# Performance work log

Measured on AMD Instinct MI355X. Metric: run time of the kernel, lower is better.

## Reference

```python
import jax, jax.numpy as jnp
import numpy as np

N = 50000      # nodes
E = 800000     # edges
F_NODE = 64    # num_node_features
F_EDGE = 16    # num_edge_features
C = 64         # out_channels
L = 3          # n_hidden_layers
G = 512        # num graphs in batch
NCLS = 10      # num_classes
EPS = 1e-5


def _lin_init(k, shape, fan_in):
    lim = 1.0 / np.sqrt(fan_in)
    return jax.random.uniform(k, shape, jnp.float32, -lim, lim)


def setup_inputs() -> dict:
    key = jax.random.key(0)
    ks = jax.random.split(key, 32)
    inp = {
        "x": jax.random.normal(ks[0], (N, F_NODE), jnp.float32),
        "edge_index": jax.random.randint(ks[1], (2, E), 0, N, jnp.int32),
        "batch": ((jnp.arange(N) * G) // N).astype(jnp.int32),  # sorted, covers all graphs
        "dropout": 0,
        "edge_attr": jax.random.uniform(ks[2], (E, F_EDGE), jnp.float32),
        # conv1: PDNConv(F_NODE, C, F_EDGE, F_EDGE). torch Linear layout [out,in].
        "c1_lw": _lin_init(ks[3], (C, F_NODE), F_NODE),
        "c1_w1": _lin_init(ks[4], (F_EDGE, F_EDGE), F_EDGE),
        "c1_b1": _lin_init(ks[5], (F_EDGE,), F_EDGE),
        "c1_w2": _lin_init(ks[6], (1, F_EDGE), F_EDGE),
        "c1_b2": _lin_init(ks[7], (1,), F_EDGE),
        # hidden_conv_1 / hidden_conv_2: L stacked PDNConv(C, C, F_EDGE, F_EDGE)
        "h1_lw": _lin_init(ks[8], (L, C, C), C),
        "h1_w1": _lin_init(ks[9], (L, F_EDGE, F_EDGE), F_EDGE),
        "h1_b1": _lin_init(ks[10], (L, F_EDGE), F_EDGE),
        "h1_w2": _lin_init(ks[11], (L, 1, F_EDGE), F_EDGE),
        "h1_b2": _lin_init(ks[12], (L, 1), F_EDGE),
        "h2_lw": _lin_init(ks[13], (L, C, C), C),
        "h2_w1": _lin_init(ks[14], (L, F_EDGE, F_EDGE), F_EDGE),
        "h2_b1": _lin_init(ks[15], (L, F_EDGE), F_EDGE),
        "h2_w2": _lin_init(ks[16], (L, 1, F_EDGE), F_EDGE),
        "h2_b2": _lin_init(ks[17], (L, 1), F_EDGE),
        # final classifier Linear(C, NCLS)
        "lin_w": _lin_init(ks[18], (NCLS, C), C),
        "lin_b": _lin_init(ks[19], (NCLS,), C),
    }
    return inp


def _pdn_conv(x, row, col, loop, edge_attr, lw, w1, b1, w2, b2):
    """PDNConv: edge-MLP weight -> add self loops -> gcn_norm -> gather-scale-scatter."""
    # edge weight MLP: Linear -> ReLU -> Linear -> Sigmoid, squeeze to [E]
    w = jax.nn.sigmoid(jnp.squeeze(jax.nn.relu(edge_attr @ w1.T + b1) @ w2.T + b2, -1))
    wf = jnp.concatenate([w, jnp.ones((x.shape[0],), x.dtype)])  # self-loop weight 1
    r = jnp.concatenate([row, loop])
    c = jnp.concatenate([col, loop])
    deg = jax.ops.segment_sum(wf, c, num_segments=x.shape[0])
    dis = jnp.where(deg > 0, 1.0 / jnp.sqrt(deg), 0.0)
    norm = dis[r] * wf * dis[c]                 # gcn_norm edge coefficients
    xl = x @ lw.T                                # node transform [N, C]
    msg = xl[r] * norm[:, None]                  # gather + scale [E+N, C]
    return jax.ops.segment_sum(msg, c, num_segments=x.shape[0])


def _batch_norm(x):
    # fresh BatchNorm each forward: weight=1, bias=0, training-mode batch stats
    mu = jnp.mean(x, axis=0)
    var = jnp.mean(jnp.square(x - mu), axis=0)  # biased var
    return (x - mu) * jax.lax.rsqrt(var + EPS)


def reference(x, edge_index, batch, dropout, edge_attr,
              c1_lw, c1_w1, c1_b1, c1_w2, c1_b2,
              h1_lw, h1_w1, h1_b1, h1_w2, h1_b2,
              h2_lw, h2_w1, h2_b1, h2_w2, h2_b2,
              lin_w, lin_b):
    row, col = edge_index[0], edge_index[1]
    loop = jnp.arange(x.shape[0], dtype=row.dtype)

    x = _pdn_conv(x, row, col, loop, edge_attr, c1_lw, c1_w1, c1_b1, c1_w2, c1_b2)
    x0 = x
    for i in range(L):
        x = jax.nn.relu(_batch_norm(x))
        x = _pdn_conv(x, row, col, loop, edge_attr,
                      h1_lw[i], h1_w1[i], h1_b1[i], h1_w2[i], h1_b2[i])
    x1 = x + x0
    x = x + x0
    for i in range(L):
        x = jax.nn.relu(_batch_norm(x))
        x = _pdn_conv(x, row, col, loop, edge_attr,
                      h2_lw[i], h2_w1[i], h2_b1[i], h2_w2[i], h2_b2[i])
    x2 = jax.nn.relu(x + x0 + x1)
    pooled = jax.ops.segment_max(x2, batch, num_segments=G)  # global max pool [G, C]
    # dropout p passed in is 0 / eval -> identity
    return pooled @ lin_w.T + lin_b
```

## Files before the change

kernel.cpp:

```cpp
#include <hip/hip_runtime.h>
#include <hip/hip_bf16.h>
#include <math.h>

#define NN 50000
#define NE 800000
#define FE 16
#define CC 64
#define NG 512
#define NCLS 10
#define NCONV 7
#define SCAN_B 49

struct MlpP { const float* w1; const float* b1; const float* w2; const float* b2; };
struct MlpAll { MlpP p[NCONV]; };

__device__ __forceinline__ int lowerb(const int* __restrict__ a, int n, int key) {
  int lo = 0, hi = n;
  while (lo < hi) { int m = (lo + hi) >> 1; if (a[m] < key) lo = m + 1; else hi = m; }
  return lo;
}

__global__ __launch_bounds__(256) void k_hist(const int* __restrict__ ecol, int* __restrict__ cnt) {
  int e = blockIdx.x * 256 + threadIdx.x;
  if (e < NE) atomicAdd(&cnt[ecol[e]], 1);
}

__global__ __launch_bounds__(1024) void k_scanA(const int* __restrict__ cnt, int* __restrict__ excl,
                                                int* __restrict__ bsum) {
  __shared__ int sc[1024];
  int t = threadIdx.x;
  int i = blockIdx.x * 1024 + t;
  int v = (i < NN) ? cnt[i] : 0;
  sc[t] = v;
  __syncthreads();
  for (int off = 1; off < 1024; off <<= 1) {
    int u = (t >= off) ? sc[t - off] : 0;
    __syncthreads();
    sc[t] += u;
    __syncthreads();
  }
  if (i < NN) excl[i] = sc[t] - v;
  if (t == 1023) bsum[blockIdx.x] = sc[1023];
}

__global__ void k_scanB(const int* __restrict__ bsum, int* __restrict__ boff) {
  int lane = threadIdx.x;
  int v = (lane < SCAN_B) ? bsum[lane] : 0;
  int own = v;
  for (int off = 1; off < 64; off <<= 1) {
    int u = __shfl_up(v, off);
    if (lane >= off) v += u;
  }
  if (lane < SCAN_B) boff[lane] = v - own;
}

__global__ __launch_bounds__(1024) void k_scanC(const int* __restrict__ excl, const int* __restrict__ boff,
                                                int* __restrict__ cptr, int* __restrict__ cursor) {
  int i = blockIdx.x * 1024 + threadIdx.x;
  if (i < NN) {
    int p = excl[i] + boff[blockIdx.x];
    cptr[i] = p;
    cursor[i] = p;
  }
  if (i == 0) cptr[NN] = NE;
}

__global__ __launch_bounds__(256) void k_scatter(
    const int* __restrict__ erow, const int* __restrict__ ecol,
    int* __restrict__ cursor, int* __restrict__ csrc, int* __restrict__ pos) {
  int e = blockIdx.x * 256 + threadIdx.x;
  if (e >= NE) return;
  int c = ecol[e];
  int p = atomicAdd(&cursor[c], 1);
  csrc[p] = erow[e];
  pos[e] = p;
}

__global__ __launch_bounds__(256) void k_mlp(
    const int* __restrict__ pos, const float* __restrict__ ea,
    float* __restrict__ wcsr8, MlpAll mw) {
  int e = blockIdx.x * 256 + threadIdx.x;
  if (e >= NE) return;
  float a[16];
  const float4* ea4 = reinterpret_cast<const float4*>(ea + (size_t)e * 16);
  float4 q0 = ea4[0], q1 = ea4[1], q2 = ea4[2], q3 = ea4[3];
  a[0]=q0.x; a[1]=q0.y; a[2]=q0.z; a[3]=q0.w;
  a[4]=q1.x; a[5]=q1.y; a[6]=q1.z; a[7]=q1.w;
  a[8]=q2.x; a[9]=q2.y; a[10]=q2.z; a[11]=q2.w;
  a[12]=q3.x; a[13]=q3.y; a[14]=q3.z; a[15]=q3.w;
  float wv[NCONV];
  #pragma unroll
  for (int j = 0; j < NCONV; ++j) {
    const float* w1 = mw.p[j].w1;
    const float* b1 = mw.p[j].b1;
    const float* w2 = mw.p[j].w2;
    float z = mw.p[j].b2[0];
    #pragma unroll
    for (int k = 0; k < 16; ++k) {
      float h = b1[k];
      #pragma unroll
      for (int m = 0; m < 16; ++m) h += a[m] * w1[k * 16 + m];
      h = h > 0.f ? h : 0.f;
      z += h * w2[k];
    }
    wv[j] = 1.f / (1.f + __expf(-z));
  }
  int p = pos[e];
  float4* dst = reinterpret_cast<float4*>(wcsr8 + (size_t)p * 8);
  dst[0] = make_float4(wv[0], wv[1], wv[2], wv[3]);
  dst[1] = make_float4(wv[4], wv[5], wv[6], 0.f);
}

__global__ __launch_bounds__(256) void k_deg(const float* __restrict__ wcsr8,
                                             const int* __restrict__ cptr,
                                             float* __restrict__ dis) {
  int n = blockIdx.x * 256 + threadIdx.x;
  if (n >= NN) return;
  int lo = cptr[n], hi = cptr[n + 1];
  float s0=0,s1=0,s2=0,s3=0,s4=0,s5=0,s6=0;
  for (int k = lo; k < hi; ++k) {
    const float4* q = reinterpret_cast<const float4*>(wcsr8 + (size_t)k * 8);
    float4 a = q[0], b = q[1];
    s0+=a.x; s1+=a.y; s2+=a.z; s3+=a.w; s4+=b.x; s5+=b.y; s6+=b.z;
  }
  dis[0*NN+n]=rsqrtf(s0+1.f); dis[1*NN+n]=rsqrtf(s1+1.f); dis[2*NN+n]=rsqrtf(s2+1.f);
  dis[3*NN+n]=rsqrtf(s3+1.f); dis[4*NN+n]=rsqrtf(s4+1.f); dis[5*NN+n]=rsqrtf(s5+1.f);
  dis[6*NN+n]=rsqrtf(s6+1.f);
}

__global__ __launch_bounds__(256) void k_lwt(const float* __restrict__ c1, const float* __restrict__ h1,
                                             const float* __restrict__ h2, float* __restrict__ lwT) {
  int id = blockIdx.x * 256 + threadIdx.x;
  if (id >= NCONV * CC * CC) return;
  int j = id >> 12;
  int r = id & 4095;
  int co = r >> 6, ci = r & 63;
  const float* src = (j == 0) ? c1 : (j <= 3 ? h1 + (j - 1) * 4096 : h2 + (j - 4) * 4096);
  lwT[j * 4096 + ci * 64 + co] = src[co * 64 + ci];
}

__global__ __launch_bounds__(256) void k_bnstat(const float* __restrict__ src, float* __restrict__ accum) {
  __shared__ float sS[256], sQ[256];
  int t = threadIdx.x;
  int c = t & 63, rg = t >> 6;
  int base = blockIdx.x * 196;
  float S = 0.f, Q = 0.f;
  for (int rr = rg; rr < 196; rr += 4) {
    int r = base + rr;
    if (r < NN) { float v = src[r * 64 + c]; S += v; Q += v * v; }
  }
  sS[t] = S; sQ[t] = Q;
  __syncthreads();
  if (t < 128) { sS[t] += sS[t + 128]; sQ[t] += sQ[t + 128]; }
  __syncthreads();
  if (t < 64) {
    atomicAdd(&accum[c], sS[t] + sS[t + 64]);
    atomicAdd(&accum[64 + c], sQ[t] + sQ[t + 64]);
  }
}

__global__ __launch_bounds__(256) void k_gemm(const float* __restrict__ src, const float* __restrict__ lwT,
                                              const float* __restrict__ accum, const float* __restrict__ dis,
                                              float* __restrict__ dst, int useBN) {
  __shared__ float xs[64 * 65];
  int t = threadIdx.x;
  int rows0 = blockIdx.x * 64;
  for (int i = 0; i < 4; ++i) {
    int f = t + i * 256;
    int r = f >> 4, c4 = (f & 15) * 4;
    int row = rows0 + r;
    float4 v = make_float4(0.f, 0.f, 0.f, 0.f);
    if (row < NN) v = *reinterpret_cast<const float4*>(src + (size_t)row * 64 + c4);
    if (useBN) {
      float4 S = *reinterpret_cast<const float4*>(accum + c4);
      float4 Q = *reinterpret_cast<const float4*>(accum + 64 + c4);
      float mu, var, rs;
      mu = S.x * (1.0f/NN); var = Q.x*(1.0f/NN)-mu*mu; var = var<0.f?0.f:var; rs = rsqrtf(var+1e-5f);
      v.x = (v.x-mu)*rs; v.x = v.x>0.f?v.x:0.f;
      mu = S.y * (1.0f/NN); var = Q.y*(1.0f/NN)-mu*mu; var = var<0.f?0.f:var; rs = rsqrtf(var+1e-5f);
      v.y = (v.y-mu)*rs; v.y = v.y>0.f?v.y:0.f;
      mu = S.z * (1.0f/NN); var = Q.z*(1.0f/NN)-mu*mu; var = var<0.f?0.f:var; rs = rsqrtf(var+1e-5f);
      v.z = (v.z-mu)*rs; v.z = v.z>0.f?v.z:0.f;
      mu = S.w * (1.0f/NN); var = Q.w*(1.0f/NN)-mu*mu; var = var<0.f?0.f:var; rs = rsqrtf(var+1e-5f);
      v.w = (v.w-mu)*rs; v.w = v.w>0.f?v.w:0.f;
    }
    xs[r * 65 + c4 + 0] = v.x;
    xs[r * 65 + c4 + 1] = v.y;
    xs[r * 65 + c4 + 2] = v.z;
    xs[r * 65 + c4 + 3] = v.w;
  }
  __syncthreads();
  int lane = t & 63;
  int cobase = __builtin_amdgcn_readfirstlane((t >> 6) << 4);
  float acc[16];
  #pragma unroll
  for (int u = 0; u < 16; ++u) acc[u] = 0.f;
  #pragma unroll 8
  for (int ci = 0; ci < 64; ++ci) {
    float xv = xs[lane * 65 + ci];
    const float* wrow = lwT + ci * 64 + cobase;
    #pragma unroll
    for (int u = 0; u < 16; ++u) acc[u] += xv * wrow[u];
  }
  __syncthreads();
  int row = rows0 + lane;
  float d = (row < NN) ? dis[row] : 0.f;
  #pragma unroll
  for (int u = 0; u < 16; ++u) xs[lane * 65 + cobase + u] = acc[u] * d;
  __syncthreads();
  for (int i = 0; i < 4; ++i) {
    int f = t + i * 256;
    int r = f >> 4, c4 = (f & 15) * 4;
    int orow = rows0 + r;
    if (orow < NN) {
      float4 v = make_float4(xs[r*65+c4], xs[r*65+c4+1], xs[r*65+c4+2], xs[r*65+c4+3]);
      *reinterpret_cast<float4*>(dst + (size_t)orow * 64 + c4) = v;
    }
  }
}

__global__ __launch_bounds__(256) void k_agg(const float* __restrict__ T, const float* __restrict__ wj,
                                             const int* __restrict__ csrc, const int* __restrict__ cptr,
                                             const float* __restrict__ dis, float* __restrict__ out,
                                             const float* __restrict__ skipA, const float* __restrict__ skipX1,
                                             float* __restrict__ outX1, int mode) {
  int t = threadIdx.x;
  int n = blockIdx.x * 4 + (t >> 6);
  if (n >= NN) return;
  int lane = t & 63;
  int lo = cptr[n], hi = cptr[n + 1];
  float acc = T[(size_t)n * 64 + lane];
  int k = lo;
  for (; k + 3 < hi; k += 4) {
    int s0 = csrc[k], s1 = csrc[k + 1], s2 = csrc[k + 2], s3 = csrc[k + 3];
    float w0 = wj[(size_t)k * 8],       w1 = wj[(size_t)(k + 1) * 8];
    float w2 = wj[(size_t)(k + 2) * 8], w3 = wj[(size_t)(k + 3) * 8];
    float t0 = T[(size_t)s0 * 64 + lane], t1 = T[(size_t)s1 * 64 + lane];
    float t2 = T[(size_t)s2 * 64 + lane], t3 = T[(size_t)s3 * 64 + lane];
    acc += w0 * t0; acc += w1 * t1; acc += w2 * t2; acc += w3 * t3;
  }
  for (; k < hi; ++k) {
    int s0 = csrc[k];
    float w0 = wj[(size_t)k * 8];
    acc += w0 * T[(size_t)s0 * 64 + lane];
  }
  float v = dis[n] * acc;
  size_t idx = (size_t)n * 64 + lane;
  if (mode == 1) {
    float sv = v + skipA[idx];
    out[idx] = sv;
    outX1[idx] = sv;
  } else if (mode == 2) {
    float sv = v + skipA[idx] + skipX1[idx];
    out[idx] = sv > 0.f ? sv : 0.f;
  } else {
    out[idx] = v;
  }
}

__global__ void k_pool(const float* __restrict__ x2, const int* __restrict__ batch, float* __restrict__ pooled) {
  int g = blockIdx.x;
  int c = threadIdx.x;
  int lo = lowerb(batch, NN, g);
  int hi = lowerb(batch, NN, g + 1);
  float m = -INFINITY;
  for (int n = lo; n < hi; ++n) m = fmaxf(m, x2[(size_t)n * 64 + c]);
  pooled[g * 64 + c] = m;
}

__global__ __launch_bounds__(256) void k_cls(const float* __restrict__ pooled, const float* __restrict__ lw,
                                             const float* __restrict__ lb, float* __restrict__ out) {
  int id = blockIdx.x * 256 + threadIdx.x;
  if (id >= NG * NCLS) return;
  int g = id / NCLS, k = id % NCLS;
  float acc = lb[k];
  #pragma unroll 8
  for (int c = 0; c < 64; ++c) acc += pooled[g * 64 + c] * lw[k * 64 + c];
  out[id] = acc;
}

extern "C" void kernel_launch(void* const* d_in, const int* in_sizes, int n_in,
                              void* d_out, int out_size, void* d_ws, size_t ws_size,
                              hipStream_t stream) {
  (void)in_sizes; (void)n_in; (void)out_size; (void)ws_size;
  const float* x     = (const float*)d_in[0];
  const int*   ei    = (const int*)d_in[1];
  const int*   batch = (const int*)d_in[2];
  const float* ea    = (const float*)d_in[4];
  const float* c1_lw = (const float*)d_in[5];
  const float* c1_w1 = (const float*)d_in[6];
  const float* c1_b1 = (const float*)d_in[7];
  const float* c1_w2 = (const float*)d_in[8];
  const float* c1_b2 = (const float*)d_in[9];
  const float* h1_lw = (const float*)d_in[10];
  const float* h1_w1 = (const float*)d_in[11];
  const float* h1_b1 = (const float*)d_in[12];
  const float* h1_w2 = (const float*)d_in[13];
  const float* h1_b2 = (const float*)d_in[14];
  const float* h2_lw = (const float*)d_in[15];
  const float* h2_w1 = (const float*)d_in[16];
  const float* h2_b1 = (const float*)d_in[17];
  const float* h2_w2 = (const float*)d_in[18];
  const float* h2_b2 = (const float*)d_in[19];
  const float* lin_w = (const float*)d_in[20];
  const float* lin_b = (const float*)d_in[21];
  float* out = (float*)d_out;

  char* base = (char*)d_ws;
  size_t off = 0;
  auto alloc = [&](size_t bytes) -> size_t {
    size_t o = off;
    off = (off + bytes + 255) & ~(size_t)255;
    return o;
  };
  size_t o_wcsr8  = alloc((size_t)NE * 8 * 4);
  size_t o_csrc   = alloc((size_t)NE * 4);
  size_t o_pos    = alloc((size_t)NE * 4);
  size_t o_cptr   = alloc((size_t)(NN + 1) * 4);
  size_t o_excl   = alloc((size_t)NN * 4);
  size_t o_bsum   = alloc((size_t)64 * 4);
  size_t o_boff   = alloc((size_t)64 * 4);
  size_t o_cnt    = alloc((size_t)NN * 4);
  size_t o_accum  = alloc((size_t)6 * 128 * 4);
  size_t o_dis    = alloc((size_t)NCONV * NN * 4);
  size_t o_lwt    = alloc((size_t)NCONV * 4096 * 4);
  size_t o_T      = alloc((size_t)NN * 64 * 4);
  size_t o_A      = alloc((size_t)NN * 64 * 4);
  size_t o_B      = alloc((size_t)NN * 64 * 4);
  size_t o_X1     = alloc((size_t)NN * 64 * 4);
  size_t o_pool   = alloc((size_t)NG * 64 * 4);

  float* wcsr8  = (float*)(base + o_wcsr8);
  int*   csrc   = (int*)(base + o_csrc);
  int*   pos    = (int*)(base + o_pos);
  int*   cptr   = (int*)(base + o_cptr);
  int*   excl   = (int*)(base + o_excl);
  int*   bsum   = (int*)(base + o_bsum);
  int*   boff   = (int*)(base + o_boff);
  int*   cnt    = (int*)(base + o_cnt);
  float* accum  = (float*)(base + o_accum);
  float* dis    = (float*)(base + o_dis);
  float* lwt    = (float*)(base + o_lwt);
  float* T      = (float*)(base + o_T);
  float* A      = (float*)(base + o_A);
  float* B      = (float*)(base + o_B);
  float* X1     = (float*)(base + o_X1);
  float* pooled = (float*)(base + o_pool);

  hipMemsetAsync(base + o_cnt, 0, o_dis - o_cnt, stream);

  const int* erow = ei;
  const int* ecol = ei + NE;

  k_hist<<<(NE + 255) / 256, 256, 0, stream>>>(ecol, cnt);
  k_scanA<<<SCAN_B, 1024, 0, stream>>>(cnt, excl, bsum);
  k_scanB<<<1, 64, 0, stream>>>(bsum, boff);
  k_scanC<<<SCAN_B, 1024, 0, stream>>>(excl, boff, cptr, cnt);
  k_scatter<<<(NE + 255) / 256, 256, 0, stream>>>(erow, ecol, cnt, csrc, pos);

  MlpAll mw;
  mw.p[0] = {c1_w1, c1_b1, c1_w2, c1_b2};
  for (int i = 0; i < 3; ++i) {
    mw.p[1 + i] = {h1_w1 + i * 256, h1_b1 + i * 16, h1_w2 + i * 16, h1_b2 + i};
    mw.p[4 + i] = {h2_w1 + i * 256, h2_b1 + i * 16, h2_w2 + i * 16, h2_b2 + i};
  }
  k_mlp<<<(NE + 255) / 256, 256, 0, stream>>>(pos, ea, wcsr8, mw);
  k_deg<<<(NN + 255) / 256, 256, 0, stream>>>(wcsr8, cptr, dis);
  k_lwt<<<(NCONV * 4096) / 256, 256, 0, stream>>>(c1_lw, h1_lw, h2_lw, lwt);

  const int GB = (NN + 63) / 64;
  const int AB = (NN + 3) / 4;

  k_gemm<<<GB, 256, 0, stream>>>(x, lwt, nullptr, dis, T, 0);
  k_agg<<<AB, 256, 0, stream>>>(T, wcsr8 + 0, csrc, cptr, dis, A, nullptr, nullptr, nullptr, 0);

  for (int i = 0; i < 3; ++i) {
    const float* src = (i == 0) ? A : B;
    k_bnstat<<<256, 256, 0, stream>>>(src, accum + i * 128);
    k_gemm<<<GB, 256, 0, stream>>>(src, lwt + (1 + i) * 4096, accum + i * 128,
                                   dis + (size_t)(1 + i) * NN, T, 1);
    int mode = (i == 2) ? 1 : 0;
    k_agg<<<AB, 256, 0, stream>>>(T, wcsr8 + (1 + i), csrc, cptr,
                                  dis + (size_t)(1 + i) * NN, B, A, nullptr, X1, mode);
  }
  for (int i = 0; i < 3; ++i) {
    k_bnstat<<<256, 256, 0, stream>>>(B, accum + (3 + i) * 128);
    k_gemm<<<GB, 256, 0, stream>>>(B, lwt + (4 + i) * 4096, accum + (3 + i) * 128,
                                   dis + (size_t)(4 + i) * NN, T, 1);
    int mode = (i == 2) ? 2 : 0;
    k_agg<<<AB, 256, 0, stream>>>(T, wcsr8 + (4 + i), csrc, cptr,
                                  dis + (size_t)(4 + i) * NN, B, A, X1, nullptr, mode);
  }

  k_pool<<<NG, 64, 0, stream>>>(B, batch, pooled);
  k_cls<<<(NG * NCLS + 255) / 256, 256, 0, stream>>>(pooled, lin_w, lin_b, out);
}
```

Before: 702.7 us.

## Fuse max-pool into final aggregation, unroll gather, process two edges per MLP thread

The separate pooling kernel is removed. The last aggregation now applies ReLU and does an integer atomicMax straight into a zeroed pooled buffer, which is valid because the values are non-negative after ReLU. Mode 1 now writes only X1 instead of both B and X1, and the next layer reads X1. The edge MLP handles two edges per thread so the weight loads are shared, and the gather loop is unrolled to 8 to keep more loads in flight. The cost is contended atomics on 512×64 pooled entries and higher register pressure in the MLP kernel.

Result: faster. 662.8 us (-5.7%).

```diff
diff --git a/kernel.cpp b/kernel.cpp
--- a/kernel.cpp
+++ b/kernel.cpp
@@ -13,12 +13,6 @@
 
 struct MlpP { const float* w1; const float* b1; const float* w2; const float* b2; };
 struct MlpAll { MlpP p[NCONV]; };
-
-__device__ __forceinline__ int lowerb(const int* __restrict__ a, int n, int key) {
-  int lo = 0, hi = n;
-  while (lo < hi) { int m = (lo + hi) >> 1; if (a[m] < key) lo = m + 1; else hi = m; }
-  return lo;
-}
 
 __global__ __launch_bounds__(256) void k_hist(const int* __restrict__ ecol, int* __restrict__ cnt) {
   int e = blockIdx.x * 256 + threadIdx.x;
@@ -79,36 +73,53 @@
 __global__ __launch_bounds__(256) void k_mlp(
     const int* __restrict__ pos, const float* __restrict__ ea,
     float* __restrict__ wcsr8, MlpAll mw) {
-  int e = blockIdx.x * 256 + threadIdx.x;
-  if (e >= NE) return;
-  float a[16];
-  const float4* ea4 = reinterpret_cast<const float4*>(ea + (size_t)e * 16);
-  float4 q0 = ea4[0], q1 = ea4[1], q2 = ea4[2], q3 = ea4[3];
-  a[0]=q0.x; a[1]=q0.y; a[2]=q0.z; a[3]=q0.w;
-  a[4]=q1.x; a[5]=q1.y; a[6]=q1.z; a[7]=q1.w;
-  a[8]=q2.x; a[9]=q2.y; a[10]=q2.z; a[11]=q2.w;
-  a[12]=q3.x; a[13]=q3.y; a[14]=q3.z; a[15]=q3.w;
-  float wv[NCONV];
+  int ep = blockIdx.x * 256 + threadIdx.x;
+  if (ep >= NE / 2) return;
+  int e0 = ep * 2;
+  float a[2][16];
+  #pragma unroll
+  for (int t = 0; t < 2; ++t) {
+    const float4* ea4 = reinterpret_cast<const float4*>(ea + (size_t)(e0 + t) * 16);
+    float4 q0 = ea4[0], q1 = ea4[1], q2 = ea4[2], q3 = ea4[3];
+    a[t][0]=q0.x; a[t][1]=q0.y; a[t][2]=q0.z; a[t][3]=q0.w;
+    a[t][4]=q1.x; a[t][5]=q1.y; a[t][6]=q1.z; a[t][7]=q1.w;
+    a[t][8]=q2.x; a[t][9]=q2.y; a[t][10]=q2.z; a[t][11]=q2.w;
+    a[t][12]=q3.x; a[t][13]=q3.y; a[t][14]=q3.z; a[t][15]=q3.w;
+  }
+  int2 pp = *reinterpret_cast<const int2*>(pos + e0);
+  float wv[2][NCONV];
   #pragma unroll
   for (int j = 0; j < NCONV; ++j) {
     const float* w1 = mw.p[j].w1;
     const float* b1 = mw.p[j].b1;
     const float* w2 = mw.p[j].w2;
-    float z = mw.p[j].b2[0];
+    float b2v = mw.p[j].b2[0];
+    float z0 = b2v, z1 = b2v;
     #pragma unroll
     for (int k = 0; k < 16; ++k) {
-      float h = b1[k];
+      float bk = b1[k];
+      float wk = w2[k];
+      float h0 = bk, h1 = bk;
       #pragma unroll
-      for (int m = 0; m < 16; ++m) h += a[m] * w1[k * 16 + m];
-      h = h > 0.f ? h : 0.f;
-      z += h * w2[k];
+      for (int m = 0; m < 16; ++m) {
+        float wm = w1[k * 16 + m];
+        h0 += a[0][m] * wm;
+        h1 += a[1][m] * wm;
+      }
+      h0 = h0 > 0.f ? h0 : 0.f;
+      h1 = h1 > 0.f ? h1 : 0.f;
+      z0 += h0 * wk;
+      z1 += h1 * wk;
     }
-    wv[j] = 1.f / (1.f + __expf(-z));
-  }
-  int p = pos[e];
-  float4* dst = reinterpret_cast<float4*>(wcsr8 + (size_t)p * 8);
-  dst[0] = make_float4(wv[0], wv[1], wv[2], wv[3]);
-  dst[1] = make_float4(wv[4], wv[5], wv[6], 0.f);
+    wv[0][j] = 1.f / (1.f + __expf(-z0));
+    wv[1][j] = 1.f / (1.f + __expf(-z1));
+  }
+  float4* d0 = reinterpret_cast<float4*>(wcsr8 + (size_t)pp.x * 8);
+  d0[0] = make_float4(wv[0][0], wv[0][1], wv[0][2], wv[0][3]);
+  d0[1] = make_float4(wv[0][4], wv[0][5], wv[0][6], 0.f);
+  float4* d1 = reinterpret_cast<float4*>(wcsr8 + (size_t)pp.y * 8);
+  d1[0] = make_float4(wv[1][0], wv[1][1], wv[1][2], wv[1][3]);
+  d1[1] = make_float4(wv[1][4], wv[1][5], wv[1][6], 0.f);
 }
 
 __global__ __launch_bounds__(256) void k_deg(const float* __restrict__ wcsr8,
@@ -223,7 +234,8 @@
                                              const int* __restrict__ csrc, const int* __restrict__ cptr,
                                              const float* __restrict__ dis, float* __restrict__ out,
                                              const float* __restrict__ skipA, const float* __restrict__ skipX1,
-                                             float* __restrict__ outX1, int mode) {
+                                             float* __restrict__ outX1, const int* __restrict__ batch,
+                                             int* __restrict__ poolI, int mode) {
   int t = threadIdx.x;
   int n = blockIdx.x * 4 + (t >> 6);
   if (n >= NN) return;
@@ -231,13 +243,21 @@
   int lo = cptr[n], hi = cptr[n + 1];
   float acc = T[(size_t)n * 64 + lane];
   int k = lo;
-  for (; k + 3 < hi; k += 4) {
-    int s0 = csrc[k], s1 = csrc[k + 1], s2 = csrc[k + 2], s3 = csrc[k + 3];
-    float w0 = wj[(size_t)k * 8],       w1 = wj[(size_t)(k + 1) * 8];
-    float w2 = wj[(size_t)(k + 2) * 8], w3 = wj[(size_t)(k + 3) * 8];
-    float t0 = T[(size_t)s0 * 64 + lane], t1 = T[(size_t)s1 * 64 + lane];
-    float t2 = T[(size_t)s2 * 64 + lane], t3 = T[(size_t)s3 * 64 + lane];
-    acc += w0 * t0; acc += w1 * t1; acc += w2 * t2; acc += w3 * t3;
+  for (; k + 8 <= hi; k += 8) {
+    int s0=csrc[k+0], s1=csrc[k+1], s2=csrc[k+2], s3=csrc[k+3];
+    int s4=csrc[k+4], s5=csrc[k+5], s6=csrc[k+6], s7=csrc[k+7];
+    float w0=wj[(size_t)(k+0)*8], w1=wj[(size_t)(k+1)*8], w2=wj[(size_t)(k+2)*8], w3=wj[(size_t)(k+3)*8];
+    float w4=wj[(size_t)(k+4)*8], w5=wj[(size_t)(k+5)*8], w6=wj[(size_t)(k+6)*8], w7=wj[(size_t)(k+7)*8];
+    float t0=T[(size_t)s0*64+lane], t1=T[(size_t)s1*64+lane], t2=T[(size_t)s2*64+lane], t3=T[(size_t)s3*64+lane];
+    float t4=T[(size_t)s4*64+lane], t5=T[(size_t)s5*64+lane], t6=T[(size_t)s6*64+lane], t7=T[(size_t)s7*64+lane];
+    acc += w0*t0; acc += w1*t1; acc += w2*t2; acc += w3*t3;
+    acc += w4*t4; acc += w5*t5; acc += w6*t6; acc += w7*t7;
+  }
+  for (; k + 4 <= hi; k += 4) {
+    int s0=csrc[k+0], s1=csrc[k+1], s2=csrc[k+2], s3=csrc[k+3];
+    float w0=wj[(size_t)(k+0)*8], w1=wj[(size_t)(k+1)*8], w2=wj[(size_t)(k+2)*8], w3=wj[(size_t)(k+3)*8];
+    float t0=T[(size_t)s0*64+lane], t1=T[(size_t)s1*64+lane], t2=T[(size_t)s2*64+lane], t3=T[(size_t)s3*64+lane];
+    acc += w0*t0; acc += w1*t1; acc += w2*t2; acc += w3*t3;
   }
   for (; k < hi; ++k) {
     int s0 = csrc[k];
@@ -247,25 +267,15 @@
   float v = dis[n] * acc;
   size_t idx = (size_t)n * 64 + lane;
   if (mode == 1) {
-    float sv = v + skipA[idx];
-    out[idx] = sv;
-    outX1[idx] = sv;
+    outX1[idx] = v + skipA[idx];
   } else if (mode == 2) {
     float sv = v + skipA[idx] + skipX1[idx];
-    out[idx] = sv > 0.f ? sv : 0.f;
+    sv = sv > 0.f ? sv : 0.f;
+    int g = batch[n];
+    atomicMax(&poolI[(size_t)g * 64 + lane], __float_as_int(sv));
   } else {
     out[idx] = v;
   }
-}
-
-__global__ void k_pool(const float* __restrict__ x2, const int* __restrict__ batch, float* __restrict__ pooled) {
-  int g = blockIdx.x;
-  int c = threadIdx.x;
-  int lo = lowerb(batch, NN, g);
-  int hi = lowerb(batch, NN, g + 1);
-  float m = -INFINITY;
-  for (int n = lo; n < hi; ++n) m = fmaxf(m, x2[(size_t)n * 64 + c]);
-  pooled[g * 64 + c] = m;
 }
 
 __global__ __launch_bounds__(256) void k_cls(const float* __restrict__ pooled, const float* __restrict__ lw,
@@ -348,6 +358,7 @@
   float* pooled = (float*)(base + o_pool);
 
   hipMemsetAsync(base + o_cnt, 0, o_dis - o_cnt, stream);
+  hipMemsetAsync(base + o_pool, 0, (size_t)NG * 64 * 4, stream);
 
   const int* erow = ei;
   const int* ecol = ei + NE;
@@ -364,7 +375,7 @@
     mw.p[1 + i] = {h1_w1 + i * 256, h1_b1 + i * 16, h1_w2 + i * 16, h1_b2 + i};
     mw.p[4 + i] = {h2_w1 + i * 256, h2_b1 + i * 16, h2_w2 + i * 16, h2_b2 + i};
   }
-  k_mlp<<<(NE + 255) / 256, 256, 0, stream>>>(pos, ea, wcsr8, mw);
+  k_mlp<<<(NE / 2 + 255) / 256, 256, 0, stream>>>(pos, ea, wcsr8, mw);
   k_deg<<<(NN + 255) / 256, 256, 0, stream>>>(wcsr8, cptr, dis);
   k_lwt<<<(NCONV * 4096) / 256, 256, 0, stream>>>(c1_lw, h1_lw, h2_lw, lwt);
 
@@ -372,7 +383,8 @@
   const int AB = (NN + 3) / 4;
 
   k_gemm<<<GB, 256, 0, stream>>>(x, lwt, nullptr, dis, T, 0);
-  k_agg<<<AB, 256, 0, stream>>>(T, wcsr8 + 0, csrc, cptr, dis, A, nullptr, nullptr, nullptr, 0);
+  k_agg<<<AB, 256, 0, stream>>>(T, wcsr8 + 0, csrc, cptr, dis, A,
+                                nullptr, nullptr, nullptr, nullptr, nullptr, 0);
 
   for (int i = 0; i < 3; ++i) {
     const float* src = (i == 0) ? A : B;
@@ -381,17 +393,19 @@
                                    dis + (size_t)(1 + i) * NN, T, 1);
     int mode = (i == 2) ? 1 : 0;
     k_agg<<<AB, 256, 0, stream>>>(T, wcsr8 + (1 + i), csrc, cptr,
-                                  dis + (size_t)(1 + i) * NN, B, A, nullptr, X1, mode);
+                                  dis + (size_t)(1 + i) * NN, B, A, nullptr, X1,
+                                  nullptr, nullptr, mode);
   }
   for (int i = 0; i < 3; ++i) {
-    k_bnstat<<<256, 256, 0, stream>>>(B, accum + (3 + i) * 128);
-    k_gemm<<<GB, 256, 0, stream>>>(B, lwt + (4 + i) * 4096, accum + (3 + i) * 128,
+    const float* src = (i == 0) ? X1 : B;
+    k_bnstat<<<256, 256, 0, stream>>>(src, accum + (3 + i) * 128);
+    k_gemm<<<GB, 256, 0, stream>>>(src, lwt + (4 + i) * 4096, accum + (3 + i) * 128,
                                    dis + (size_t)(4 + i) * NN, T, 1);
     int mode = (i == 2) ? 2 : 0;
     k_agg<<<AB, 256, 0, stream>>>(T, wcsr8 + (4 + i), csrc, cptr,
-                                  dis + (size_t)(4 + i) * NN, B, A, X1, nullptr, mode);
-  }
-
-  k_pool<<<NG, 64, 0, stream>>>(B, batch, pooled);
+                                  dis + (size_t)(4 + i) * NN, B, A, X1, nullptr,
+                                  batch, (int*)pooled, mode);
+  }
+
   k_cls<<<(NG * NCLS + 255) / 256, 256, 0, stream>>>(pooled, lin_w, lin_b, out);
 }
```
